# Performance work log

Measured on AMD Instinct MI355X. Metric: run time of the kernel, lower is better.

The kernel has to match this reference:

```python
import jax, jax.numpy as jnp
import numpy as np

N_QUBITS = 10
DEPTH = 6


def _ry(theta):
    # RY(theta) = [[cos(t/2), -sin(t/2)], [sin(t/2), cos(t/2)]]
    c = jnp.cos(theta / 2)
    s = jnp.sin(theta / 2)
    return jnp.stack([jnp.stack([c, -s]), jnp.stack([s, c])]).astype(jnp.complex64)


def _rot(phi, theta, omega):
    # PennyLane Rot(phi, theta, omega) = RZ(omega) RY(theta) RZ(phi)
    c = jnp.cos(theta / 2)
    s = jnp.sin(theta / 2)
    ep = jnp.exp(-0.5j * (phi + omega).astype(jnp.complex64))
    em = jnp.exp(-0.5j * (phi - omega).astype(jnp.complex64))
    return jnp.stack([
        jnp.stack([ep * c, -jnp.conj(em) * s]),
        jnp.stack([em * s, jnp.conj(ep) * c]),
    ])


def _apply_1q(psi, U, w):
    # psi: (2,)*n statevector; apply 2x2 unitary U on qubit axis w
    psi = jnp.tensordot(U, psi, axes=([1], [w]))
    return jnp.moveaxis(psi, 0, w)


def _apply_cnot(psi, c, t):
    # flip target axis t on the control=1 slice of axis c
    psi = jnp.moveaxis(psi, (c, t), (0, 1))
    psi = jnp.concatenate([psi[:1], psi[1:, ::-1]], axis=0)
    return jnp.moveaxis(psi, (0, 1), (c, t))


def _circuit(angles, weights):
    """RY encoding + StronglyEntanglingLayers + PauliZ expvals. angles: (n,), weights: (depth, n, 3)."""
    n = N_QUBITS
    psi = jnp.zeros((2,) * n, jnp.complex64).at[(0,) * n].set(1.0)
    for i in range(n):
        psi = _apply_1q(psi, _ry(angles[i]), i)
    for l in range(DEPTH):
        for i in range(n):
            psi = _apply_1q(psi, _rot(weights[l, i, 0], weights[l, i, 1], weights[l, i, 2]), i)
        r = (l % (n - 1)) + 1  # default StronglyEntanglingLayers range schedule
        for i in range(n):
            psi = _apply_cnot(psi, i, (i + r) % n)
    p = psi.real ** 2 + psi.imag ** 2  # probabilities, shape (2,)*n
    exps = []
    for i in range(n):
        pm = jnp.moveaxis(p, i, 0).reshape(2, -1).sum(axis=1)
        exps.append(pm[0] - pm[1])  # <Z_i>
    return jnp.stack(exps)


def setup_inputs() -> dict:
    key = jax.random.key(0)
    ks = jax.random.split(key, 5)
    B, F, C = 8192, 1024, 10
    x = jax.random.normal(ks[0], (B, F), jnp.float32)
    W_proj = jax.random.normal(ks[1], (N_QUBITS, F), jnp.float32) / np.sqrt(F).astype(np.float32)
    weights = 0.01 * jax.random.normal(ks[2], (DEPTH, N_QUBITS, 3), jnp.float32)
    W_out = jax.random.normal(ks[3], (C, N_QUBITS), jnp.float32) / np.sqrt(N_QUBITS).astype(np.float32)
    b_out = 0.01 * jax.random.normal(ks[4], (C,), jnp.float32)
    return {"x": x, "W_proj": W_proj, "weights": weights, "W_out": W_out, "b_out": b_out}


def reference(x, W_proj, weights, W_out, b_out):
    # classical projection + angle encoding
    angles = jnp.tanh(x @ W_proj.T) * jnp.float32(np.pi / 2)  # (B, n_qubits)
    # batched exact statevector simulation of the VQC
    q = jax.vmap(_circuit, in_axes=(0, None))(angles, weights)  # (B, n_qubits)
    return q @ W_out.T + b_out  # (B, num_classes)
```

## Files before the change

kernel.cpp:

```cpp
#include <hip/hip_runtime.h>
#include <math.h>
#include <stdint.h>

#define NQ 10
#define DEPTH 6

typedef _Float16 f16x8 __attribute__((ext_vector_type(8)));
typedef float f32x4 __attribute__((ext_vector_type(4)));

typedef __attribute__((address_space(3))) unsigned int lds_u32;
typedef const __attribute__((address_space(1))) unsigned int glb_u32;

__device__ __forceinline__ void async_load16(const unsigned short* g, unsigned short* l) {
    __builtin_amdgcn_global_load_lds((glb_u32*)g, (lds_u32*)l, 16, 0, 0);
}

__device__ __forceinline__ void compute_gate(const float* __restrict__ weights,
                                             int idx, float* __restrict__ g) {
    float phi   = weights[idx * 3 + 0];
    float theta = weights[idx * 3 + 1];
    float omega = weights[idx * 3 + 2];
    float c = cosf(0.5f * theta), s = sinf(0.5f * theta);
    float ap = -0.5f * (phi + omega);
    float am = -0.5f * (phi - omega);
    float epr = cosf(ap), epi = sinf(ap);
    float emr = cosf(am), emi = sinf(am);
    g[0] =  epr * c;  g[1] =  epi * c;
    g[2] = -emr * s;  g[3] =  emi * s;
    g[4] =  emr * s;  g[5] =  emi * s;
    g[6] =  epr * c;  g[7] = -epi * c;
}

__global__ void prep_gates_kernel(const float* __restrict__ weights,
                                  float* __restrict__ gmat) {
    int idx = blockIdx.x * blockDim.x + threadIdx.x;
    if (idx >= DEPTH * NQ) return;
    compute_gate(weights, idx, gmat + idx * 8);
}

__device__ __forceinline__ void apply_1q_local(
    float (&ar)[16], float (&ai)[16], int q,
    float u00r, float u00i, float u01r, float u01i,
    float u10r, float u10i, float u11r, float u11i) {
#pragma unroll
    for (int j = 0; j < 16; ++j) {
        if ((j >> q) & 1) continue;
        int j1 = j | (1 << q);
        float a0r = ar[j],  a0i = ai[j];
        float a1r = ar[j1], a1i = ai[j1];
        ar[j]  = u00r*a0r - u00i*a0i + u01r*a1r - u01i*a1i;
        ai[j]  = u00r*a0i + u00i*a0r + u01r*a1i + u01i*a1r;
        ar[j1] = u10r*a0r - u10i*a0i + u11r*a1r - u11i*a1i;
        ai[j1] = u10r*a0i + u10i*a0r + u11r*a1i + u11i*a1r;
    }
}

__device__ __forceinline__ void apply_1q_lane(
    float (&ar)[16], float (&ai)[16], int q, int lane,
    float u00r, float u00i, float u01r, float u01i,
    float u10r, float u10i, float u11r, float u11i) {
    int  m  = 1 << (q - 4);
    bool hi = (lane >> (q - 4)) & 1;
    float car = hi ? u11r : u00r, cai = hi ? u11i : u00i;
    float cbr = hi ? u10r : u01r, cbi = hi ? u10i : u01i;
    float pr[16], pi[16];
#pragma unroll
    for (int j = 0; j < 16; ++j) pr[j] = __shfl_xor(ar[j], m, 64);
#pragma unroll
    for (int j = 0; j < 16; ++j) pi[j] = __shfl_xor(ai[j], m, 64);
#pragma unroll
    for (int j = 0; j < 16; ++j) {
        float mr = ar[j], mi = ai[j];
        ar[j] = car*mr - cai*mi + cbr*pr[j] - cbi*pi[j];
        ai[j] = car*mi + cai*mr + cbr*pi[j] + cbi*pr[j];
    }
}

__device__ __forceinline__ void cnot_gate(
    float (&ar)[16], float (&ai)[16], int c, int t, int lane) {
    if (c < 4 && t < 4) {
#pragma unroll
        for (int j = 0; j < 16; ++j) {
            if (((j >> c) & 1) && !((j >> t) & 1)) {
                int j1 = j | (1 << t);
                float tr = ar[j]; ar[j] = ar[j1]; ar[j1] = tr;
                float ti = ai[j]; ai[j] = ai[j1]; ai[j1] = ti;
            }
        }
    } else if (c < 4) {
        int m = 1 << (t - 4);
        float pr[16], pi[16];
#pragma unroll
        for (int j = 0; j < 16; ++j)
            if ((j >> c) & 1) pr[j] = __shfl_xor(ar[j], m, 64);
#pragma unroll
        for (int j = 0; j < 16; ++j)
            if ((j >> c) & 1) pi[j] = __shfl_xor(ai[j], m, 64);
#pragma unroll
        for (int j = 0; j < 16; ++j)
            if ((j >> c) & 1) { ar[j] = pr[j]; ai[j] = pi[j]; }
    } else if (t < 4) {
        bool cb = (lane >> (c - 4)) & 1;
#pragma unroll
        for (int j = 0; j < 16; ++j) {
            if (!((j >> t) & 1)) {
                int j1 = j | (1 << t);
                float lr = ar[j], li = ai[j], hr = ar[j1], hi2 = ai[j1];
                ar[j]  = cb ? hr : lr;  ai[j]  = cb ? hi2 : li;
                ar[j1] = cb ? lr : hr;  ai[j1] = cb ? li : hi2;
            }
        }
    } else {
        int  m  = 1 << (t - 4);
        bool cb = (lane >> (c - 4)) & 1;
        float pr[16], pi[16];
#pragma unroll
        for (int j = 0; j < 16; ++j) pr[j] = __shfl_xor(ar[j], m, 64);
#pragma unroll
        for (int j = 0; j < 16; ++j) pi[j] = __shfl_xor(ai[j], m, 64);
#pragma unroll
        for (int j = 0; j < 16; ++j) {
            ar[j] = cb ? pr[j] : ar[j];
            ai[j] = cb ? pi[j] : ai[j];
        }
    }
}

template <int R>
__device__ __forceinline__ void cnot_ring(float (&ar)[16], float (&ai)[16], int lane) {
#pragma unroll
    for (int i = 0; i < NQ; ++i) cnot_gate(ar, ai, i, (i + R) % NQ, lane);
}

template <int R>
__device__ __forceinline__ void cnot_ring_rev(float (&ar)[16], float (&ai)[16], int lane) {
#pragma unroll
    for (int i = NQ - 1; i >= 0; --i) cnot_gate(ar, ai, i, (i + R) % NQ, lane);
}

__device__ __forceinline__ void run_circuit(float (&ar)[16], float (&ai)[16],
                                            const float* __restrict__ gmat, int lane) {
    for (int l = 0; l < DEPTH; ++l) {
        const float* gl = gmat + l * (NQ * 8);
#pragma unroll
        for (int i = 0; i < NQ; ++i) {
            const float* g = gl + i * 8;
            float u00r = g[0], u00i = g[1], u01r = g[2], u01i = g[3];
            float u10r = g[4], u10i = g[5], u11r = g[6], u11i = g[7];
            if (i < 4)
                apply_1q_local(ar, ai, i, u00r,u00i,u01r,u01i,u10r,u10i,u11r,u11i);
            else
                apply_1q_lane(ar, ai, i, lane, u00r,u00i,u01r,u01i,u10r,u10i,u11r,u11i);
        }
        switch (l) {
            case 0: cnot_ring<1>(ar, ai, lane); break;
            case 1: cnot_ring<2>(ar, ai, lane); break;
            case 2: cnot_ring<3>(ar, ai, lane); break;
            case 3: cnot_ring<4>(ar, ai, lane); break;
            case 4: cnot_ring<5>(ar, ai, lane); break;
            default: cnot_ring<6>(ar, ai, lane); break;
        }
    }
}

__device__ __forceinline__ void run_circuit_T(float (&ar)[16], float (&ai)[16],
                                              const float* __restrict__ gmat, int lane) {
    for (int l = DEPTH - 1; l >= 0; --l) {
        switch (l) {
            case 0: cnot_ring_rev<1>(ar, ai, lane); break;
            case 1: cnot_ring_rev<2>(ar, ai, lane); break;
            case 2: cnot_ring_rev<3>(ar, ai, lane); break;
            case 3: cnot_ring_rev<4>(ar, ai, lane); break;
            case 4: cnot_ring_rev<5>(ar, ai, lane); break;
            default: cnot_ring_rev<6>(ar, ai, lane); break;
        }
        const float* gl = gmat + l * (NQ * 8);
#pragma unroll
        for (int i = 0; i < NQ; ++i) {
            const float* g = gl + i * 8;
            float u00r = g[0], u00i = g[1];
            float u01r = g[4], u01i = g[5];
            float u10r = g[2], u10i = g[3];
            float u11r = g[6], u11i = g[7];
            if (i < 4)
                apply_1q_local(ar, ai, i, u00r,u00i,u01r,u01i,u10r,u10i,u11r,u11i);
            else
                apply_1q_lane(ar, ai, i, lane, u00r,u00i,u01r,u01i,u10r,u10i,u11r,u11i);
        }
    }
}

__device__ __forceinline__ float wave_sum(float v) {
#pragma unroll
    for (int m = 1; m < 64; m <<= 1) v += __shfl_xor(v, m, 64);
    return v;
}

__device__ __forceinline__ void proj_v_body(
    const float* __restrict__ x, const float* __restrict__ Wproj,
    _Float16* __restrict__ V, int b, int lane) {
    const float* xb = x + (size_t)b * 1024;
    float acc[NQ];
#pragma unroll
    for (int q = 0; q < NQ; ++q) acc[q] = 0.f;
#pragma unroll
    for (int k = 0; k < 16; ++k) {
        float xv = xb[k * 64 + lane];
#pragma unroll
        for (int q = 0; q < NQ; ++q)
            acc[q] = fmaf(xv, Wproj[q * 1024 + k * 64 + lane], acc[q]);
    }
#pragma unroll
    for (int q = 0; q < NQ; ++q) acc[q] = wave_sum(acc[q]);

    float cq[NQ], sq[NQ];
#pragma unroll
    for (int q = 0; q < NQ; ++q) {
        float ang = tanhf(acc[q]) * 1.57079632679489662f;
        cq[q] = cosf(0.5f * ang);
        sq[q] = sinf(0.5f * ang);
    }
    float laneprod = 1.f;
#pragma unroll
    for (int q = 4; q < NQ; ++q)
        laneprod *= ((lane >> (q - 4)) & 1) ? sq[q] : cq[q];

    unsigned int buf[8];
#pragma unroll
    for (int jj = 0; jj < 8; ++jj) {
        unsigned short h2[2];
#pragma unroll
        for (int c = 0; c < 2; ++c) {
            int j = jj * 2 + c;
            float p = laneprod;
#pragma unroll
            for (int q = 0; q < 4; ++q) p *= ((j >> q) & 1) ? sq[q] : cq[q];
            h2[c] = __builtin_bit_cast(unsigned short, (_Float16)p);
        }
        buf[jj] = (unsigned int)h2[0] | ((unsigned int)h2[1] << 16);
    }
    uint4* dst = (uint4*)(V + (size_t)b * 1024 + 16 * lane);
    uint4 v0; v0.x = buf[0]; v0.y = buf[1]; v0.z = buf[2]; v0.w = buf[3];
    uint4 v1; v1.x = buf[4]; v1.y = buf[5]; v1.z = buf[6]; v1.w = buf[7];
    dst[0] = v0; dst[1] = v1;
}

__global__ __launch_bounds__(256) void basis_proj_kernel(
    const float* __restrict__ weights, _Float16* __restrict__ Bt,
    const float* __restrict__ x, const float* __restrict__ Wproj,
    _Float16* __restrict__ V, int B) {
    __shared__ float gmat_s[DEPTH * NQ * 8];
    int tid  = threadIdx.x;
    int lane = tid & 63;
    int w    = tid >> 6;

    if (blockIdx.x < 256) {
        if (tid < DEPTH * NQ) compute_gate(weights, tid, gmat_s + tid * 8);
        __syncthreads();

        int g = blockIdx.x * 4 + w;
        float ar[16], ai[16];
#pragma unroll
        for (int jj = 0; jj < 16; ++jj) {
            ar[jj] = (lane == (g >> 4) && jj == (g & 15)) ? 1.f : 0.f;
            ai[jj] = 0.f;
        }
        run_circuit_T(ar, ai, gmat_s, lane);

        unsigned int bufr[8], bufi[8];
#pragma unroll
        for (int jj = 0; jj < 8; ++jj) {
            unsigned short r0 = __builtin_bit_cast(unsigned short, (_Float16)ar[2*jj]);
            unsigned short r1 = __builtin_bit_cast(unsigned short, (_Float16)ar[2*jj+1]);
            unsigned short i0 = __builtin_bit_cast(unsigned short, (_Float16)ai[2*jj]);
            unsigned short i1 = __builtin_bit_cast(unsigned short, (_Float16)ai[2*jj+1]);
            bufr[jj] = (unsigned int)r0 | ((unsigned int)r1 << 16);
            bufi[jj] = (unsigned int)i0 | ((unsigned int)i1 << 16);
        }
        uint4* dre = (uint4*)((unsigned short*)Bt + (size_t)(2*g)     * 1024 + 16 * lane);
        uint4* dim = (uint4*)((unsigned short*)Bt + (size_t)(2*g + 1) * 1024 + 16 * lane);
        uint4 v;
        v.x = bufr[0]; v.y = bufr[1]; v.z = bufr[2]; v.w = bufr[3]; dre[0] = v;
        v.x = bufr[4]; v.y = bufr[5]; v.z = bufr[6]; v.w = bufr[7]; dre[1] = v;
        v.x = bufi[0]; v.y = bufi[1]; v.z = bufi[2]; v.w = bufi[3]; dim[0] = v;
        v.x = bufi[4]; v.y = bufi[5]; v.z = bufi[6]; v.w = bufi[7]; dim[1] = v;
    } else {
        int b = (blockIdx.x - 256) * 4 + w;
        if (b < B) proj_v_body(x, Wproj, V, b, lane);
    }
}

__device__ __forceinline__ void gemm_tile_body(
    unsigned short* As, unsigned short* Bs,
    const unsigned short* __restrict__ A, const unsigned short* __restrict__ Bt,
    float* __restrict__ Zpart, int m0, int n0, int nb, int tid) {
    int lane = tid & 63;
    int w    = tid >> 6;
    int mh   = (w >> 1) * 64, nh = (w & 1) * 64;
    int quad = lane >> 4;
    int lrow = lane & 15;
    int srow  = (lane >> 3);
    int schnk = (lane & 7) ^ srow;

    f32x4 acc[4][4];
#pragma unroll
    for (int mi = 0; mi < 4; ++mi)
#pragma unroll
        for (int ni = 0; ni < 4; ++ni)
            acc[mi][ni] = (f32x4){0.f, 0.f, 0.f, 0.f};

    for (int kt = 0; kt < 16; ++kt) {
        if (kt) __syncthreads();
#pragma unroll
        for (int r = 0; r < 4; ++r) {
            int s   = w * 4 + r;
            int row = s * 8 + srow;
            async_load16(A  + (size_t)(m0 + row) * 1024 + kt * 64 + schnk * 8,
                         As + s * 512);
            async_load16(Bt + (size_t)(n0 + row) * 1024 + kt * 64 + schnk * 8,
                         Bs + s * 512);
        }
        asm volatile("s_waitcnt vmcnt(0)" ::: "memory");
        __syncthreads();
#pragma unroll
        for (int kk = 0; kk < 2; ++kk) {
            f16x8 af[4], bf[4];
#pragma unroll
            for (int i = 0; i < 4; ++i) {
                int cxa = (kk * 4 + quad) ^ (lrow & 7);
                af[i] = *(const f16x8*)(As + (mh + i * 16 + lrow) * 64 + cxa * 8);
                bf[i] = *(const f16x8*)(Bs + (nh + i * 16 + lrow) * 64 + cxa * 8);
            }
#pragma unroll
            for (int mi = 0; mi < 4; ++mi)
#pragma unroll
                for (int ni = 0; ni < 4; ++ni)
                    acc[mi][ni] = __builtin_amdgcn_mfma_f32_16x16x32_f16(
                        af[mi], bf[ni], acc[mi][ni], 0, 0, 0);
        }
    }

    __syncthreads();
    float* Zs = (float*)As;
#pragma unroll
    for (int mi = 0; mi < 4; ++mi) {
#pragma unroll
        for (int r = 0; r < 4; ++r) {
            float p0 = acc[mi][0][r] * acc[mi][0][r];
            float p1 = acc[mi][1][r] * acc[mi][1][r];
            float p2 = acc[mi][2][r] * acc[mi][2][r];
            float p3 = acc[mi][3][r] * acc[mi][3][r];
            float t0 = (p0 + p1) + (p2 + p3);
            float t3 = (p0 - p1) + (p2 - p3);
            float t4 = (p0 + p1) - (p2 + p3);
            t0 += __shfl_xor(t0, 1, 64);
            t3 += __shfl_xor(t3, 1, 64);
            t4 += __shfl_xor(t4, 1, 64);
            float u2 = __shfl_xor(t0, 2, 64);
            float ap = t0 + u2;
            float am = (lane & 2) ? u2 - t0 : t0 - u2;
            t3 += __shfl_xor(t3, 2, 64);
            t4 += __shfl_xor(t4, 2, 64);
            float u4  = __shfl_xor(ap, 4, 64);
            float bpp = ap + u4;
            float bpm = (lane & 4) ? u4 - ap : ap - u4;
            float bmp = am + __shfl_xor(am, 4, 64);
            t3 += __shfl_xor(t3, 4, 64);
            t4 += __shfl_xor(t4, 4, 64);
            float u8 = __shfl_xor(bpp, 8, 64);
            float T  = bpp + u8;
            float Z2 = (lane & 8) ? u8 - bpp : bpp - u8;
            float Z1 = bpm + __shfl_xor(bpm, 8, 64);
            float Z0 = bmp + __shfl_xor(bmp, 8, 64);
            t3 += __shfl_xor(t3, 8, 64);
            t4 += __shfl_xor(t4, 8, 64);
            if (lrow == 0) {
                int row = mh + mi * 16 + quad * 4 + r;
                float* z = Zs + ((size_t)(w & 1) * 128 + row) * 8;
                z[0] = T;  z[1] = Z0; z[2] = Z1; z[3] = Z2;
                z[4] = t3; z[5] = t4;
            }
        }
    }
    __syncthreads();
    {
        int row  = tid >> 1, part = tid & 1;
        const float* za = Zs + (size_t)row * 8;
        const float* zb = Zs + (size_t)(128 + row) * 8;
        float o[4];
        if (part == 0) {
            o[0] = za[0] + zb[0];
            o[1] = za[1] + zb[1];
            o[2] = za[2] + zb[2];
            o[3] = za[3] + zb[3];
        } else {
            o[0] = za[4] + zb[4];
            o[1] = za[5] + zb[5];
            o[2] = za[0] - zb[0];
            o[3] = 0.f;
        }
        float4 v = {o[0], o[1], o[2], o[3]};
        *(float4*)(Zpart + ((size_t)(m0 + row) * 16 + nb) * 8 + part * 4) = v;
    }
}

__global__ __launch_bounds__(256) void gemm_fused_kernel(
    const unsigned short* __restrict__ A, const unsigned short* __restrict__ Bt,
    float* __restrict__ Zpart) {
    __shared__ unsigned short As[128 * 64];
    __shared__ unsigned short Bs[128 * 64];
    gemm_tile_body(As, Bs, A, Bt, Zpart,
                   blockIdx.x * 128, blockIdx.y * 128, blockIdx.y, threadIdx.x);
}

__device__ __forceinline__ void combine_head_body(
    const float* __restrict__ Zpart, const float* __restrict__ Wout,
    const float* __restrict__ bout, float* __restrict__ out, int b, int lane) {
    float z[8];
    if (lane < 16) {
        const float4* p = (const float4*)(Zpart + ((size_t)b * 16 + lane) * 8);
        float4 a = p[0], c = p[1];
        z[0]=a.x; z[1]=a.y; z[2]=a.z; z[3]=a.w; z[4]=c.x; z[5]=c.y; z[6]=c.z; z[7]=c.w;
    } else {
#pragma unroll
        for (int i = 0; i < 8; ++i) z[i] = 0.f;
    }
    float Zq[NQ];
#pragma unroll
    for (int q = 0; q < 6; ++q) {
        float v = z[q + 1];
        v += __shfl_xor(v, 1, 64);
        v += __shfl_xor(v, 2, 64);
        v += __shfl_xor(v, 4, 64);
        v += __shfl_xor(v, 8, 64);
        Zq[q] = v;
    }
    {
        float T = z[0];
        float u1 = __shfl_xor(T, 1, 64);
        float P  = T + u1;
        float M  = (lane & 1) ? u1 - T : T - u1;
        float u2 = __shfl_xor(P, 2, 64);
        float PP = P + u2;
        float PM = (lane & 2) ? u2 - P : P - u2;
        float MP = M + __shfl_xor(M, 2, 64);
        float u4  = __shfl_xor(PP, 4, 64);
        float PPP = PP + u4;
        float PPM = (lane & 4) ? u4 - PP : PP - u4;
        float PMP = PM + __shfl_xor(PM, 4, 64);
        float MPP = MP + __shfl_xor(MP, 4, 64);
        float u8 = __shfl_xor(PPP, 8, 64);
        Zq[9] = (lane & 8) ? u8 - PPP : PPP - u8;
        Zq[8] = PPM + __shfl_xor(PPM, 8, 64);
        Zq[7] = PMP + __shfl_xor(PMP, 8, 64);
        Zq[6] = MPP + __shfl_xor(MPP, 8, 64);
    }
    if (lane < NQ) {
        float o = bout[lane];
#pragma unroll
        for (int q = 0; q < NQ; ++q) o = fmaf(Zq[q], Wout[lane * NQ + q], o);
        out[(size_t)b * NQ + lane] = o;
    }
}

__global__ __launch_bounds__(256) void combine_head_kernel(
    const float* __restrict__ Zpart, const float* __restrict__ Wout,
    const float* __restrict__ bout, float* __restrict__ out, int B) {
    int lane = threadIdx.x & 63;
    int wid  = threadIdx.x >> 6;
    int b    = blockIdx.x * 4 + wid;
    if (b >= B) return;
    combine_head_body(Zpart, Wout, bout, out, b, lane);
}

__global__ __launch_bounds__(256) void vqc_kernel(
    const float* __restrict__ x, const float* __restrict__ Wproj,
    const float* __restrict__ gmat, const float* __restrict__ Wout,
    const float* __restrict__ bout, float* __restrict__ out, int B) {
    int lane = threadIdx.x & 63;
    int wid  = threadIdx.x >> 6;
    int b    = blockIdx.x * 4 + wid;
    if (b >= B) return;

    const float* xb = x + (size_t)b * 1024;
    float acc[NQ];
#pragma unroll
    for (int q = 0; q < NQ; ++q) acc[q] = 0.f;
#pragma unroll
    for (int k = 0; k < 16; ++k) {
        float xv = xb[k * 64 + lane];
#pragma unroll
        for (int q = 0; q < NQ; ++q)
            acc[q] = fmaf(xv, Wproj[q * 1024 + k * 64 + lane], acc[q]);
    }
#pragma unroll
    for (int q = 0; q < NQ; ++q) acc[q] = wave_sum(acc[q]);

    float cq[NQ], sq[NQ];
#pragma unroll
    for (int q = 0; q < NQ; ++q) {
        float ang = tanhf(acc[q]) * 1.57079632679489662f;
        cq[q] = cosf(0.5f * ang);
        sq[q] = sinf(0.5f * ang);
    }
    float laneprod = 1.f;
#pragma unroll
    for (int q = 4; q < NQ; ++q)
        laneprod *= ((lane >> (q - 4)) & 1) ? sq[q] : cq[q];
    float ar[16], ai[16];
#pragma unroll
    for (int j = 0; j < 16; ++j) {
        float p = laneprod;
#pragma unroll
        for (int q = 0; q < 4; ++q) p *= ((j >> q) & 1) ? sq[q] : cq[q];
        ar[j] = p; ai[j] = 0.f;
    }
    run_circuit(ar, ai, gmat, lane);

    float T = 0.f, S[4] = {0.f, 0.f, 0.f, 0.f};
#pragma unroll
    for (int j = 0; j < 16; ++j) {
        float p = ar[j] * ar[j] + ai[j] * ai[j];
        T += p;
#pragma unroll
        for (int q = 0; q < 4; ++q) S[q] += ((j >> q) & 1) ? -p : p;
    }
    float Zq[NQ];
#pragma unroll
    for (int q = 0; q < 4; ++q) Zq[q] = S[q];
#pragma unroll
    for (int q = 4; q < NQ; ++q) Zq[q] = ((lane >> (q - 4)) & 1) ? -T : T;
#pragma unroll
    for (int q = 0; q < NQ; ++q) Zq[q] = wave_sum(Zq[q]);
    if (lane < NQ) {
        float o = bout[lane];
#pragma unroll
        for (int q = 0; q < NQ; ++q) o = fmaf(Zq[q], Wout[lane * NQ + q], o);
        out[(size_t)b * NQ + lane] = o;
    }
}

extern "C" void kernel_launch(void* const* d_in, const int* in_sizes, int n_in,
                              void* d_out, int out_size, void* d_ws, size_t ws_size,
                              hipStream_t stream) {
    const float* x       = (const float*)d_in[0];
    const float* Wproj   = (const float*)d_in[1];
    const float* weights = (const float*)d_in[2];
    const float* Wout    = (const float*)d_in[3];
    const float* bout    = (const float*)d_in[4];
    float* out = (float*)d_out;
    int B = in_sizes[0] / 1024;

    char* ws = (char*)d_ws;
    size_t off_Bt = 4096;
    size_t off_V  = off_Bt + (size_t)2048 * 1024 * 2;
    size_t off_Z  = off_V  + (size_t)B * 1024 * 2;
    size_t need   = off_Z  + (size_t)B * 16 * 8 * 4;

    if (ws_size >= need && (B % 128) == 0) {
        _Float16* Bt = (_Float16*)(ws + off_Bt);
        _Float16* V  = (_Float16*)(ws + off_V);
        float*  Zprt = (float*)(ws + off_Z);

        basis_proj_kernel<<<256 + B / 4, 256, 0, stream>>>(weights, Bt, x, Wproj, V, B);
        gemm_fused_kernel<<<dim3(B / 128, 16), 256, 0, stream>>>(
            (const unsigned short*)V, (const unsigned short*)Bt, Zprt);
        combine_head_kernel<<<B / 4, 256, 0, stream>>>(Zprt, Wout, bout, out, B);
    } else {
        float* gmat = (float*)ws;
        prep_gates_kernel<<<1, 64, 0, stream>>>(weights, gmat);
        vqc_kernel<<<(B + 3) / 4, 256, 0, stream>>>(x, Wproj, gmat, Wout, bout, out, B);
    }
}
```

Baseline: 164.3 us.

## Fuse output head into GEMM epilogue via atomics, drop combine kernel

Removes the separate combine_head kernel and the Zpart workspace. Each GEMM tile now builds its partial Z expectation values, applies the W_out head using weights staged in shared memory, and atomically adds its contribution into the output. The output is first filled with the bias by 40 extra blocks appended to the basis/projection kernel. This saves one kernel launch and the Zpart write/read round trip, at the cost of 16 atomic adds per output element and a changed summation order in floating point. The shared-memory Z stride also changes from 8 to 9.

```diff
diff --git a/kernel.cpp b/kernel.cpp
--- a/kernel.cpp
+++ b/kernel.cpp
@@ -248,11 +248,13 @@
 __global__ __launch_bounds__(256) void basis_proj_kernel(
     const float* __restrict__ weights, _Float16* __restrict__ Bt,
     const float* __restrict__ x, const float* __restrict__ Wproj,
-    _Float16* __restrict__ V, int B) {
+    _Float16* __restrict__ V, const float* __restrict__ bout,
+    float* __restrict__ out, int B) {
     __shared__ float gmat_s[DEPTH * NQ * 8];
     int tid  = threadIdx.x;
     int lane = tid & 63;
     int w    = tid >> 6;
+    int nproj = B / 4;
 
     if (blockIdx.x < 256) {
         if (tid < DEPTH * NQ) compute_gate(weights, tid, gmat_s + tid * 8);
@@ -284,23 +286,38 @@
         v.x = bufr[4]; v.y = bufr[5]; v.z = bufr[6]; v.w = bufr[7]; dre[1] = v;
         v.x = bufi[0]; v.y = bufi[1]; v.z = bufi[2]; v.w = bufi[3]; dim[0] = v;
         v.x = bufi[4]; v.y = bufi[5]; v.z = bufi[6]; v.w = bufi[7]; dim[1] = v;
-    } else {
+    } else if (blockIdx.x < 256 + nproj) {
         int b = (blockIdx.x - 256) * 4 + w;
         if (b < B) proj_v_body(x, Wproj, V, b, lane);
-    }
-}
-
-__device__ __forceinline__ void gemm_tile_body(
-    unsigned short* As, unsigned short* Bs,
-    const unsigned short* __restrict__ A, const unsigned short* __restrict__ Bt,
-    float* __restrict__ Zpart, int m0, int n0, int nb, int tid) {
+    } else {
+        int t0 = (blockIdx.x - 256 - nproj) * 256 + tid;
+        int n  = B * NQ;
+        for (int i = t0; i < n; i += 40 * 256)
+            out[i] = bout[i % NQ];
+    }
+}
+
+__global__ __launch_bounds__(256) void gemm_fused_kernel(
+    const unsigned short* __restrict__ A,
+    const unsigned short* __restrict__ Bt,
+    const float* __restrict__ Wout,
+    float* __restrict__ out) {
+    __shared__ unsigned short As[128 * 64];
+    __shared__ unsigned short Bs[128 * 64];
+    __shared__ float WoutS[NQ * NQ];
+    int tid  = threadIdx.x;
     int lane = tid & 63;
     int w    = tid >> 6;
+    int m0   = blockIdx.x * 128;
+    int nb   = blockIdx.y;
+    int n0   = nb * 128;
     int mh   = (w >> 1) * 64, nh = (w & 1) * 64;
     int quad = lane >> 4;
     int lrow = lane & 15;
     int srow  = (lane >> 3);
     int schnk = (lane & 7) ^ srow;
+
+    if (tid < NQ * NQ) WoutS[tid] = Wout[tid];
 
     f32x4 acc[4][4];
 #pragma unroll
@@ -376,101 +393,38 @@
             t4 += __shfl_xor(t4, 8, 64);
             if (lrow == 0) {
                 int row = mh + mi * 16 + quad * 4 + r;
-                float* z = Zs + ((size_t)(w & 1) * 128 + row) * 8;
+                float* z = Zs + ((size_t)(w & 1) * 128 + row) * 9;
                 z[0] = T;  z[1] = Z0; z[2] = Z1; z[3] = Z2;
                 z[4] = t3; z[5] = t4;
             }
         }
     }
     __syncthreads();
-    {
-        int row  = tid >> 1, part = tid & 1;
-        const float* za = Zs + (size_t)row * 8;
-        const float* zb = Zs + (size_t)(128 + row) * 8;
-        float o[4];
-        if (part == 0) {
-            o[0] = za[0] + zb[0];
-            o[1] = za[1] + zb[1];
-            o[2] = za[2] + zb[2];
-            o[3] = za[3] + zb[3];
-        } else {
-            o[0] = za[4] + zb[4];
-            o[1] = za[5] + zb[5];
-            o[2] = za[0] - zb[0];
-            o[3] = 0.f;
-        }
-        float4 v = {o[0], o[1], o[2], o[3]};
-        *(float4*)(Zpart + ((size_t)(m0 + row) * 16 + nb) * 8 + part * 4) = v;
-    }
-}
-
-__global__ __launch_bounds__(256) void gemm_fused_kernel(
-    const unsigned short* __restrict__ A, const unsigned short* __restrict__ Bt,
-    float* __restrict__ Zpart) {
-    __shared__ unsigned short As[128 * 64];
-    __shared__ unsigned short Bs[128 * 64];
-    gemm_tile_body(As, Bs, A, Bt, Zpart,
-                   blockIdx.x * 128, blockIdx.y * 128, blockIdx.y, threadIdx.x);
-}
-
-__device__ __forceinline__ void combine_head_body(
-    const float* __restrict__ Zpart, const float* __restrict__ Wout,
-    const float* __restrict__ bout, float* __restrict__ out, int b, int lane) {
-    float z[8];
-    if (lane < 16) {
-        const float4* p = (const float4*)(Zpart + ((size_t)b * 16 + lane) * 8);
-        float4 a = p[0], c = p[1];
-        z[0]=a.x; z[1]=a.y; z[2]=a.z; z[3]=a.w; z[4]=c.x; z[5]=c.y; z[6]=c.z; z[7]=c.w;
-    } else {
-#pragma unroll
-        for (int i = 0; i < 8; ++i) z[i] = 0.f;
-    }
-    float Zq[NQ];
-#pragma unroll
-    for (int q = 0; q < 6; ++q) {
-        float v = z[q + 1];
-        v += __shfl_xor(v, 1, 64);
-        v += __shfl_xor(v, 2, 64);
-        v += __shfl_xor(v, 4, 64);
-        v += __shfl_xor(v, 8, 64);
-        Zq[q] = v;
-    }
-    {
-        float T = z[0];
-        float u1 = __shfl_xor(T, 1, 64);
-        float P  = T + u1;
-        float M  = (lane & 1) ? u1 - T : T - u1;
-        float u2 = __shfl_xor(P, 2, 64);
-        float PP = P + u2;
-        float PM = (lane & 2) ? u2 - P : P - u2;
-        float MP = M + __shfl_xor(M, 2, 64);
-        float u4  = __shfl_xor(PP, 4, 64);
-        float PPP = PP + u4;
-        float PPM = (lane & 4) ? u4 - PP : PP - u4;
-        float PMP = PM + __shfl_xor(PM, 4, 64);
-        float MPP = MP + __shfl_xor(MP, 4, 64);
-        float u8 = __shfl_xor(PPP, 8, 64);
-        Zq[9] = (lane & 8) ? u8 - PPP : PPP - u8;
-        Zq[8] = PPM + __shfl_xor(PPM, 8, 64);
-        Zq[7] = PMP + __shfl_xor(PMP, 8, 64);
-        Zq[6] = MPP + __shfl_xor(MPP, 8, 64);
-    }
-    if (lane < NQ) {
-        float o = bout[lane];
-#pragma unroll
-        for (int q = 0; q < NQ; ++q) o = fmaf(Zq[q], Wout[lane * NQ + q], o);
-        out[(size_t)b * NQ + lane] = o;
-    }
-}
-
-__global__ __launch_bounds__(256) void combine_head_kernel(
-    const float* __restrict__ Zpart, const float* __restrict__ Wout,
-    const float* __restrict__ bout, float* __restrict__ out, int B) {
-    int lane = threadIdx.x & 63;
-    int wid  = threadIdx.x >> 6;
-    int b    = blockIdx.x * 4 + wid;
-    if (b >= B) return;
-    combine_head_body(Zpart, Wout, bout, out, b, lane);
+    if (tid < 128) {
+        int row = tid;
+        const float* za = Zs + (size_t)row * 9;
+        const float* zb = Zs + (size_t)(128 + row) * 9;
+        float T = za[0] + zb[0];
+        float Zq[NQ];
+        Zq[0] = za[1] + zb[1];
+        Zq[1] = za[2] + zb[2];
+        Zq[2] = za[3] + zb[3];
+        Zq[3] = za[4] + zb[4];
+        Zq[4] = za[5] + zb[5];
+        Zq[5] = za[0] - zb[0];
+        Zq[6] = (nb & 1) ? -T : T;
+        Zq[7] = (nb & 2) ? -T : T;
+        Zq[8] = (nb & 4) ? -T : T;
+        Zq[9] = (nb & 8) ? -T : T;
+        float* op = out + (size_t)(m0 + row) * NQ;
+#pragma unroll
+        for (int c = 0; c < NQ; ++c) {
+            float o = 0.f;
+#pragma unroll
+            for (int q = 0; q < NQ; ++q) o = fmaf(Zq[q], WoutS[c * NQ + q], o);
+            atomicAdd(op + c, o);
+        }
+    }
 }
 
 __global__ __launch_bounds__(256) void vqc_kernel(
@@ -554,18 +508,16 @@
     char* ws = (char*)d_ws;
     size_t off_Bt = 4096;
     size_t off_V  = off_Bt + (size_t)2048 * 1024 * 2;
-    size_t off_Z  = off_V  + (size_t)B * 1024 * 2;
-    size_t need   = off_Z  + (size_t)B * 16 * 8 * 4;
+    size_t need   = off_V + (size_t)B * 1024 * 2;
 
     if (ws_size >= need && (B % 128) == 0) {
         _Float16* Bt = (_Float16*)(ws + off_Bt);
         _Float16* V  = (_Float16*)(ws + off_V);
-        float*  Zprt = (float*)(ws + off_Z);
-
-        basis_proj_kernel<<<256 + B / 4, 256, 0, stream>>>(weights, Bt, x, Wproj, V, B);
+
+        basis_proj_kernel<<<256 + B / 4 + 40, 256, 0, stream>>>(
+            weights, Bt, x, Wproj, V, bout, out, B);
         gemm_fused_kernel<<<dim3(B / 128, 16), 256, 0, stream>>>(
-            (const unsigned short*)V, (const unsigned short*)Bt, Zprt);
-        combine_head_kernel<<<B / 4, 256, 0, stream>>>(Zprt, Wout, bout, out, B);
+            (const unsigned short*)V, (const unsigned short*)Bt, Wout, out);
     } else {
         float* gmat = (float*)ws;
         prep_gates_kernel<<<1, 64, 0, stream>>>(weights, gmat);
```

Result: slower. 188.4 us (+14.7%).
